# Kernel tuning notes

Measured on AMD Instinct MI355X. Metric: run time of the kernel, lower is better.

The kernel has to match this reference:

```python
import jax, jax.numpy as jnp
import numpy as np

POOL = 7
IMG = 1024.0
NUM_CLASSES = 2
R = 1000


def crop_and_resize(feat, boxes, pool):
    # feat: [C,H,W]; boxes: [N,4] normalized (y1,x1,y2,x2); returns [N,C,pool,pool]
    C, H, W = feat.shape
    y1, x1, y2, x2 = boxes[:, 0], boxes[:, 1], boxes[:, 2], boxes[:, 3]
    t = jnp.arange(pool, dtype=feat.dtype) / (pool - 1)
    ys = (y1[:, None] + (y2 - y1)[:, None] * t[None, :]) * (H - 1)  # [N,P]
    xs = (x1[:, None] + (x2 - x1)[:, None] * t[None, :]) * (W - 1)  # [N,P]
    vy = (ys >= 0) & (ys <= H - 1)
    vx = (xs >= 0) & (xs <= W - 1)
    yf = jnp.floor(ys)
    xf = jnp.floor(xs)
    wy = (ys - yf)[None, :, :, None]  # [1,N,P,1]
    wx = (xs - xf)[None, :, None, :]  # [1,N,1,P]
    y0 = jnp.clip(yf, 0, H - 1).astype(jnp.int32)
    y1i = jnp.clip(yf + 1, 0, H - 1).astype(jnp.int32)
    x0 = jnp.clip(xf, 0, W - 1).astype(jnp.int32)
    x1i = jnp.clip(xf + 1, 0, W - 1).astype(jnp.int32)

    def g(yi, xi):  # gather -> [C,N,P,P]
        return feat[:, yi[:, :, None], xi[:, None, :]]

    val = (g(y0, x0) * (1 - wy) * (1 - wx)
           + g(y0, x1i) * (1 - wy) * wx
           + g(y1i, x0) * wy * (1 - wx)
           + g(y1i, x1i) * wy * wx)
    mask = (vy[:, :, None] & vx[:, None, :])[None]  # extrapolation value 0
    return jnp.where(mask, val, 0.0).transpose(1, 0, 2, 3)


def roi_align(feats, rois_flat):
    # rois_flat: [N,4] in pixel coords (x1,y1,x2,y2)
    x1, y1, x2, y2 = rois_flat[:, 0], rois_flat[:, 1], rois_flat[:, 2], rois_flat[:, 3]
    lvl = jnp.log2(jnp.sqrt((y2 - y1) * (x2 - x1)) / 224.0)
    lvl = jnp.clip(jnp.round(lvl) + 4, 2, 5)
    boxes = rois_flat[:, jnp.array([1, 0, 3, 2])] / IMG  # (y1,x1,y2,x2) normalized
    crops = jnp.stack([crop_and_resize(f[0], boxes, POOL) for f in feats])  # [4,N,C,P,P]
    sel = (lvl[None, :] == jnp.arange(2, 6, dtype=lvl.dtype)[:, None])       # [4,N]
    return jnp.sum(jnp.where(sel[:, :, None, None, None], crops, 0.0), axis=0)  # [N,C,P,P]


def setup_inputs() -> dict:
    key = jax.random.key(0)
    ks = jax.random.split(key, 24)
    feat2 = jax.random.normal(ks[0], (1, 256, 256, 256), jnp.float32)
    feat3 = jax.random.normal(ks[1], (1, 256, 128, 128), jnp.float32)
    feat4 = jax.random.normal(ks[2], (1, 256, 64, 64), jnp.float32)
    feat5 = jax.random.normal(ks[3], (1, 256, 32, 32), jnp.float32)
    x1 = jax.random.uniform(ks[4], (1, R), minval=0.0, maxval=900.0)
    y1 = jax.random.uniform(ks[5], (1, R), minval=0.0, maxval=900.0)
    w = jax.random.uniform(ks[6], (1, R), minval=16.0, maxval=400.0)
    h = jax.random.uniform(ks[7], (1, R), minval=16.0, maxval=400.0)
    rois = jnp.stack([x1, y1, jnp.minimum(x1 + w, 1023.0), jnp.minimum(y1 + h, 1023.0)], axis=-1)
    s = 0.02
    params = dict(
        conv_w=s * jax.random.normal(ks[8], (1024, 256, POOL, POOL), jnp.float32),
        conv_b=jnp.zeros((1024,), jnp.float32),
        bn_gamma=jnp.ones((1024,), jnp.float32),
        bn_beta=jnp.zeros((1024,), jnp.float32),
        bn_mean=jnp.zeros((1024,), jnp.float32),
        bn_var=jnp.ones((1024,), jnp.float32),
        fc1_w=s * jax.random.normal(ks[9], (1024, 1024), jnp.float32),
        fc1_b=jnp.zeros((1024,), jnp.float32),
        fc2_w=s * jax.random.normal(ks[10], (1024, 1024), jnp.float32),
        fc2_b=jnp.zeros((1024,), jnp.float32),
        cls_w=s * jax.random.normal(ks[11], (NUM_CLASSES, 1024), jnp.float32),
        cls_b=jnp.zeros((NUM_CLASSES,), jnp.float32),
        bbox_w=s * jax.random.normal(ks[12], (NUM_CLASSES * 4, 1024), jnp.float32),
        bbox_b=jnp.zeros((NUM_CLASSES * 4,), jnp.float32),
    )
    return dict(feat2=feat2, feat3=feat3, feat4=feat4, feat5=feat5, rois=rois, **params)


def reference(feat2, feat3, feat4, feat5, rois, conv_w, conv_b, bn_gamma, bn_beta,
              bn_mean, bn_var, fc1_w, fc1_b, fc2_w, fc2_b, cls_w, cls_b, bbox_w, bbox_b):
    roi_number = rois.shape[1]
    pooled = roi_align([feat2, feat3, feat4, feat5], rois.reshape(-1, 4))  # [N,256,7,7]
    # conv1 (7x7 valid on 7x7 input -> 1x1 spatial) + BN (inference stats, eps=1e-3)
    y = jnp.einsum('nchw,ochw->no', pooled, conv_w) + conv_b
    y = (y - bn_mean) / jnp.sqrt(bn_var + 1e-3) * bn_gamma + bn_beta
    h = jax.nn.relu(y @ fc1_w.T + fc1_b)
    h = jax.nn.relu(h @ fc2_w.T + fc2_b)
    logits = h @ cls_w.T + cls_b
    probs = jax.nn.softmax(logits, axis=-1)
    bbox = h @ bbox_w.T + bbox_b
    return (logits.reshape(1, roi_number, NUM_CLASSES),
            probs.reshape(1, roi_number, NUM_CLASSES),
            bbox.reshape(1, roi_number, NUM_CLASSES, 4))
```

## Files before the change

### kernel.cpp

```cpp
#include <hip/hip_runtime.h>
#include <cstdint>
#include <cstddef>

typedef __attribute__((ext_vector_type(8))) short bf16x8;
typedef __attribute__((ext_vector_type(4))) float f32x4;

#define POOLK 12544

#define TOFF2 0
#define TOFF3 16777216
#define TOFF4 20971520
#define TOFF5 22020096

__device__ __forceinline__ void gld16(const void* g, void* l) {
    __builtin_amdgcn_global_load_lds(
        (const __attribute__((address_space(1))) void*)g,
        (__attribute__((address_space(3))) void*)l, 16, 0, 0);
}
__device__ __forceinline__ unsigned short f32_to_bf16(float f) {
    union { float f; unsigned u; } x; x.f = f;
    return (unsigned short)((x.u + 0x7FFFu + ((x.u >> 16) & 1u)) >> 16);
}
__device__ __forceinline__ float bf16_to_f32(unsigned short s) {
    return __uint_as_float(((unsigned)s) << 16);
}

__global__ __launch_bounds__(256) void prep_kernel(
    const float* __restrict__ f2, const float* __restrict__ f3,
    const float* __restrict__ f4, const float* __restrict__ f5,
    unsigned short* __restrict__ T,
    const float* __restrict__ conv_w, unsigned short* __restrict__ convw_bf,
    const float* __restrict__ fc1_w, unsigned short* __restrict__ fc1w_bf,
    const float* __restrict__ fc2_w, unsigned short* __restrict__ fc2w_bf,
    int do_feat)
{
    __shared__ __align__(16) unsigned short sh[8192];
    const int t = threadIdx.x;
    int b = blockIdx.x;

    if (b < 2720) {
        if (!do_feat) return;
        const float* src; unsigned short* dst; int P;
        if (b < 2048)      { src = f2; dst = T + TOFF2; P = 65536; }
        else if (b < 2560) { src = f3; dst = T + TOFF3; P = 16384; b -= 2048; }
        else if (b < 2688) { src = f4; dst = T + TOFF4; P = 4096;  b -= 2560; }
        else               { src = f5; dst = T + TOFF5; P = 1024;  b -= 2688; }
        const int p0 = b * 32;
        const int cr = t >> 3, x4 = (t & 7) * 4;
#pragma unroll
        for (int cc = 0; cc < 8; ++cc) {
            const int c = cc * 32 + cr;
            const float4 v = *(const float4*)(src + (size_t)c * P + p0 + x4);
            const int blk = c >> 3, cl = c & 7;
            float vv[4] = {v.x, v.y, v.z, v.w};
#pragma unroll
            for (int i = 0; i < 4; ++i) {
                const int p = x4 + i;
                sh[p * 256 + ((blk ^ (p >> 2)) << 3) + cl] = f32_to_bf16(vv[i]);
            }
        }
        __syncthreads();
        const int cb = t & 31;
#pragma unroll
        for (int pz = 0; pz < 4; ++pz) {
            const int pp = pz * 8 + (t >> 5);
            const bf16x8 v = *(const bf16x8*)&sh[pp * 256 + ((cb ^ (pp >> 2)) << 3)];
            *(bf16x8*)(dst + (size_t)(p0 + pp) * 256 + cb * 8) = v;
        }
        return;
    }
    b -= 2720;
    if (b < 2048) {
        const int o = b >> 1, half = b & 1;
        const float* srow = conv_w + (size_t)o * POOLK + half * 6272;
        for (int k = t; k < 6272; k += 256) sh[k] = f32_to_bf16(srow[k]);
        __syncthreads();
        unsigned short* drow = convw_bf + (size_t)o * POOLK + half * 128;
        for (int k = t; k < 6272; k += 256) {
            const int ij = k >> 7, cl = k & 127;
            drow[ij * 256 + cl] = sh[cl * 49 + ij];
        }
        return;
    }
    b -= 2048;
    {
        const float* src = (b < 1024) ? fc1_w : fc2_w;
        unsigned short* dst = (b < 1024) ? fc1w_bf : fc2w_bf;
        const int bb = b & 1023;
        const int i = (bb * 256 + t) * 4;
        const float4 v = *(const float4*)(src + i);
        ushort4 o;
        o.x = f32_to_bf16(v.x); o.y = f32_to_bf16(v.y);
        o.z = f32_to_bf16(v.z); o.w = f32_to_bf16(v.w);
        *(ushort4*)(dst + i) = o;
    }
}

__global__ __launch_bounds__(256) void roi_gather_kernel(
    const unsigned short* __restrict__ T, const float* __restrict__ rois,
    unsigned short* __restrict__ pooled, int nroi)
{
    const int n = blockIdx.x;
    const int tid = threadIdx.x;
    unsigned short* orow = pooled + (size_t)n * POOLK;
    if (n >= nroi) {
        const bf16x8 z = {};
        for (int k = tid * 8; k < POOLK; k += 2048) *(bf16x8*)(orow + k) = z;
        return;
    }
    __shared__ int sy0[7], sy1[7], sx0[7], sx1[7];
    __shared__ float swy[7], swx[7], svy[7], svx[7];

    const float rx1 = rois[n*4+0], ry1 = rois[n*4+1];
    const float rx2 = rois[n*4+2], ry2 = rois[n*4+3];
    int lvl = (int)rintf(log2f(sqrtf((ry2-ry1)*(rx2-rx1)) * (1.0f/224.0f))) + 4;
    lvl = lvl < 2 ? 2 : (lvl > 5 ? 5 : lvl);
    const int W = 256 >> (lvl - 2);
    const float Hm1 = (float)(W - 1);
    const unsigned short* Tl = T + (lvl == 2 ? TOFF2 : (lvl == 3 ? TOFF3 : (lvl == 4 ? TOFF4 : TOFF5)));

    if (tid < 7) {
        const float t = (float)tid / 6.0f;
        const float by1 = ry1*(1.0f/1024.0f), by2 = ry2*(1.0f/1024.0f);
        const float bx1 = rx1*(1.0f/1024.0f), bx2 = rx2*(1.0f/1024.0f);
        const float ys = (by1 + (by2 - by1) * t) * Hm1;
        const float xs = (bx1 + (bx2 - bx1) * t) * Hm1;
        const float yf = floorf(ys), xf = floorf(xs);
        swy[tid] = ys - yf;  swx[tid] = xs - xf;
        sy0[tid] = (int)fminf(fmaxf(yf,        0.0f), Hm1);
        sy1[tid] = (int)fminf(fmaxf(yf + 1.0f, 0.0f), Hm1);
        sx0[tid] = (int)fminf(fmaxf(xf,        0.0f), Hm1);
        sx1[tid] = (int)fminf(fmaxf(xf + 1.0f, 0.0f), Hm1);
        svy[tid] = (ys >= 0.0f && ys <= Hm1) ? 1.0f : 0.0f;
        svx[tid] = (xs >= 0.0f && xs <= Hm1) ? 1.0f : 0.0f;
    }
    __syncthreads();

    const int g  = tid >> 5;
    const int c0 = (tid & 31) * 8;
#pragma unroll
    for (int it = 0; it < 7; ++it) {
        const int pos = it * 8 + g;
        if (pos >= 49) break;
        const int i = pos / 7, j = pos % 7;
        const int y0 = sy0[i], y1 = sy1[i], x0 = sx0[j], x1 = sx1[j];
        const float wy = swy[i], wx = swx[j];
        const float scale = svy[i] * svx[j];
        const bf16x8 v00 = *(const bf16x8*)(Tl + ((size_t)(y0*W + x0))*256 + c0);
        const bf16x8 v01 = *(const bf16x8*)(Tl + ((size_t)(y0*W + x1))*256 + c0);
        const bf16x8 v10 = *(const bf16x8*)(Tl + ((size_t)(y1*W + x0))*256 + c0);
        const bf16x8 v11 = *(const bf16x8*)(Tl + ((size_t)(y1*W + x1))*256 + c0);
        bf16x8 o;
#pragma unroll
        for (int jj = 0; jj < 8; ++jj) {
            const float f00 = bf16_to_f32((unsigned short)v00[jj]);
            const float f01 = bf16_to_f32((unsigned short)v01[jj]);
            const float f10 = bf16_to_f32((unsigned short)v10[jj]);
            const float f11 = bf16_to_f32((unsigned short)v11[jj]);
            const float top = f00 + (f01 - f00) * wx;
            const float bot = f10 + (f11 - f10) * wx;
            o[jj] = (short)f32_to_bf16((top + (bot - top) * wy) * scale);
        }
        *(bf16x8*)(orow + pos * 256 + c0) = o;
    }
}

__global__ __launch_bounds__(256) void roi_direct_kernel(
    const float* __restrict__ feat2, const float* __restrict__ feat3,
    const float* __restrict__ feat4, const float* __restrict__ feat5,
    const float* __restrict__ rois, unsigned short* __restrict__ pooled, int nroi)
{
    const int n = blockIdx.x;
    const int tid = threadIdx.x;
    unsigned short* orow = pooled + (size_t)n * POOLK;
    if (n >= nroi) {
        const bf16x8 z = {};
        for (int k = tid * 8; k < POOLK; k += 2048) *(bf16x8*)(orow + k) = z;
        return;
    }
    __shared__ int sy0[7], sy1[7], sx0[7], sx1[7];
    __shared__ float swy[7], swx[7], svy[7], svx[7];
    const float rx1 = rois[n*4+0], ry1 = rois[n*4+1];
    const float rx2 = rois[n*4+2], ry2 = rois[n*4+3];
    int lvl = (int)rintf(log2f(sqrtf((ry2-ry1)*(rx2-rx1)) * (1.0f/224.0f))) + 4;
    lvl = lvl < 2 ? 2 : (lvl > 5 ? 5 : lvl);
    const int H = 256 >> (lvl - 2);
    const float Hm1 = (float)(H - 1);
    const float* feat = lvl==2 ? feat2 : (lvl==3 ? feat3 : (lvl==4 ? feat4 : feat5));
    if (tid < 7) {
        const float t = (float)tid / 6.0f;
        const float by1 = ry1*(1.0f/1024.0f), by2 = ry2*(1.0f/1024.0f);
        const float bx1 = rx1*(1.0f/1024.0f), bx2 = rx2*(1.0f/1024.0f);
        const float ys = (by1 + (by2-by1)*t) * Hm1;
        const float xs = (bx1 + (bx2-bx1)*t) * Hm1;
        const float yf = floorf(ys), xf = floorf(xs);
        swy[tid] = ys - yf;  swx[tid] = xs - xf;
        sy0[tid] = (int)fminf(fmaxf(yf,      0.0f), Hm1);
        sy1[tid] = (int)fminf(fmaxf(yf+1.0f, 0.0f), Hm1);
        sx0[tid] = (int)fminf(fmaxf(xf,      0.0f), Hm1);
        sx1[tid] = (int)fminf(fmaxf(xf+1.0f, 0.0f), Hm1);
        svy[tid] = (ys >= 0.0f && ys <= Hm1) ? 1.0f : 0.0f;
        svx[tid] = (xs >= 0.0f && xs <= Hm1) ? 1.0f : 0.0f;
    }
    __syncthreads();
    const int HW = H * H;
    for (int e = tid; e < POOLK; e += 256) {
        const int c = e / 49, ij = e % 49, i = ij / 7, j = ij % 7;
        const float* p = feat + c * HW;
        const int y0 = sy0[i], y1 = sy1[i], x0 = sx0[j], x1 = sx1[j];
        const float wy = swy[i], wx = swx[j];
        const float v00 = p[y0*H + x0], v01 = p[y0*H + x1];
        const float v10 = p[y1*H + x0], v11 = p[y1*H + x1];
        float v = v00*(1.0f-wy)*(1.0f-wx) + v01*(1.0f-wy)*wx
                + v10*wy*(1.0f-wx)        + v11*wy*wx;
        v *= svy[i] * svx[j];
        orow[ij*256 + c] = f32_to_bf16(v);
    }
}

__global__ __launch_bounds__(256, 2) void gemm_bt(
    const unsigned short* __restrict__ A, const unsigned short* __restrict__ B,
    float* __restrict__ Cpart, int K, int Kper, int nz)
{
    __shared__ __align__(16) unsigned short At[2][128*32];
    __shared__ __align__(16) unsigned short Bt[2][128*32];
    const int tid  = threadIdx.x;
    const int lane = tid & 63;
    const int bid  = blockIdx.x;
    const int z  = bid % nz;
    const int iq = bid / nz;
    const int bx = iq & 7, by = iq >> 3;
    const int wm = (tid >> 6) >> 1, wn = (tid >> 6) & 1;
    const size_t k0 = (size_t)z * Kper;

    const int r1 = tid >> 2;
    const int q  = tid & 3;
    const int csw = (q ^ (r1 & 3)) * 8;
    const unsigned short* Ag = A + ((size_t)(by * 128 + r1)) * K + k0 + csw;
    const unsigned short* Bg = B + ((size_t)(bx * 128 + r1)) * K + k0 + csw;
    const int nit = Kper >> 5;

    gld16(Ag,                  &At[0][tid * 8]);
    gld16(Ag + (size_t)64 * K, &At[0][(tid + 256) * 8]);
    gld16(Bg,                  &Bt[0][tid * 8]);
    gld16(Bg + (size_t)64 * K, &Bt[0][(tid + 256) * 8]);

    f32x4 acc[4][4] = {};
    const int fr = lane & 15;
    const int fq = lane >> 4;
    const int rslot = (fq ^ (fr & 3)) * 8;

    int buf = 0;
    for (int it = 0; it < nit; ++it) {
        if (it + 1 < nit) {
            const size_t ko = (size_t)(it + 1) * 32;
            gld16(Ag + ko,                  &At[buf ^ 1][tid * 8]);
            gld16(Ag + (size_t)64 * K + ko, &At[buf ^ 1][(tid + 256) * 8]);
            gld16(Bg + ko,                  &Bt[buf ^ 1][tid * 8]);
            gld16(Bg + (size_t)64 * K + ko, &Bt[buf ^ 1][(tid + 256) * 8]);
            asm volatile("s_waitcnt vmcnt(4)" ::: "memory");
        } else {
            asm volatile("s_waitcnt vmcnt(0)" ::: "memory");
        }
        __syncthreads();

        bf16x8 a[4], b[4];
#pragma unroll
        for (int mi = 0; mi < 4; ++mi)
            a[mi] = *(const bf16x8*)&At[buf][(wm*64 + mi*16 + fr) * 32 + rslot];
#pragma unroll
        for (int ni = 0; ni < 4; ++ni)
            b[ni] = *(const bf16x8*)&Bt[buf][(wn*64 + ni*16 + fr) * 32 + rslot];
        __builtin_amdgcn_s_setprio(1);
#pragma unroll
        for (int mi = 0; mi < 4; ++mi)
#pragma unroll
            for (int ni = 0; ni < 4; ++ni)
                acc[mi][ni] = __builtin_amdgcn_mfma_f32_16x16x32_bf16(
                    a[mi], b[ni], acc[mi][ni], 0, 0, 0);
        __builtin_amdgcn_s_setprio(0);
        __syncthreads();
        buf ^= 1;
    }

    float* Cp = Cpart + (size_t)z * (1024 * 1024);
    const int row0 = by * 128 + wm * 64;
    const int col0 = bx * 128 + wn * 64;
#pragma unroll
    for (int mi = 0; mi < 4; ++mi)
#pragma unroll
        for (int ni = 0; ni < 4; ++ni)
#pragma unroll
            for (int r = 0; r < 4; ++r)
                Cp[(size_t)(row0 + mi*16 + fq*4 + r) * 1024 + col0 + ni*16 + fr]
                    = acc[mi][ni][r];
}

__global__ void reduce_bn_kernel(const float* __restrict__ part,
    const float* __restrict__ bias, const float* __restrict__ gamma,
    const float* __restrict__ beta, const float* __restrict__ mean,
    const float* __restrict__ var, unsigned short* __restrict__ out, int nz)
{
    const int i4 = (blockIdx.x * 256 + threadIdx.x) * 4;
    const int n = i4 & 1023;
    float4 v = make_float4(0.f, 0.f, 0.f, 0.f);
    for (int zz = 0; zz < nz; ++zz) {
        const float4 p = *(const float4*)(part + (size_t)zz * 1048576 + i4);
        v.x += p.x; v.y += p.y; v.z += p.z; v.w += p.w;
    }
    const float4 bi = *(const float4*)(bias + n);
    const float4 ga = *(const float4*)(gamma + n);
    const float4 be = *(const float4*)(beta + n);
    const float4 me = *(const float4*)(mean + n);
    const float4 va = *(const float4*)(var + n);
    ushort4 o;
    o.x = f32_to_bf16((v.x + bi.x - me.x) * __frsqrt_rn(va.x + 0.001f) * ga.x + be.x);
    o.y = f32_to_bf16((v.y + bi.y - me.y) * __frsqrt_rn(va.y + 0.001f) * ga.y + be.y);
    o.z = f32_to_bf16((v.z + bi.z - me.z) * __frsqrt_rn(va.z + 0.001f) * ga.z + be.z);
    o.w = f32_to_bf16((v.w + bi.w - me.w) * __frsqrt_rn(va.w + 0.001f) * ga.w + be.w);
    *(ushort4*)(out + i4) = o;
}

__global__ __launch_bounds__(256) void gemm64_fused(
    const unsigned short* __restrict__ A, const unsigned short* __restrict__ B,
    const float* __restrict__ bias, unsigned short* __restrict__ out, int relu)
{
    __shared__ __align__(16) unsigned short At[2][64*32];
    __shared__ __align__(16) unsigned short Bt[2][64*32];
    const int tid = threadIdx.x, lane = tid & 63;
    const int w = tid >> 6, wm = w >> 1, wn = w & 1;
    const int r1 = tid >> 2;
    const int q  = tid & 3;
    const int csw = (q ^ (r1 & 3)) * 8;
    const unsigned short* Ag = A + (size_t)(blockIdx.y*64 + r1) * 1024 + csw;
    const unsigned short* Bg = B + (size_t)(blockIdx.x*64 + r1) * 1024 + csw;
    const int fr = lane & 15, fq = lane >> 4;
    const int rslot = (fq ^ (fr & 3)) * 8;

    gld16(Ag, &At[0][tid * 8]);
    gld16(Bg, &Bt[0][tid * 8]);

    f32x4 acc[2][2] = {};
    int buf = 0;
    for (int it = 0; it < 32; ++it) {
        if (it + 1 < 32) {
            const int ko = (it + 1) * 32;
            gld16(Ag + ko, &At[buf ^ 1][tid * 8]);
            gld16(Bg + ko, &Bt[buf ^ 1][tid * 8]);
            asm volatile("s_waitcnt vmcnt(2)" ::: "memory");
        } else {
            asm volatile("s_waitcnt vmcnt(0)" ::: "memory");
        }
        __syncthreads();
        bf16x8 a[2], b[2];
#pragma unroll
        for (int mi = 0; mi < 2; ++mi)
            a[mi] = *(const bf16x8*)&At[buf][(wm*32 + mi*16 + fr) * 32 + rslot];
#pragma unroll
        for (int ni = 0; ni < 2; ++ni)
            b[ni] = *(const bf16x8*)&Bt[buf][(wn*32 + ni*16 + fr) * 32 + rslot];
        __builtin_amdgcn_s_setprio(1);
#pragma unroll
        for (int mi = 0; mi < 2; ++mi)
#pragma unroll
            for (int ni = 0; ni < 2; ++ni)
                acc[mi][ni] = __builtin_amdgcn_mfma_f32_16x16x32_bf16(
                    a[mi], b[ni], acc[mi][ni], 0, 0, 0);
        __builtin_amdgcn_s_setprio(0);
        __syncthreads();
        buf ^= 1;
    }
    const int row0 = blockIdx.y*64 + wm*32;
    const int col0 = blockIdx.x*64 + wn*32;
#pragma unroll
    for (int mi = 0; mi < 2; ++mi)
#pragma unroll
        for (int ni = 0; ni < 2; ++ni)
#pragma unroll
            for (int r = 0; r < 4; ++r) {
                const int row = row0 + mi*16 + fq*4 + r;
                const int col = col0 + ni*16 + fr;
                float v = acc[mi][ni][r] + bias[col];
                if (relu) v = fmaxf(v, 0.0f);
                out[(size_t)row * 1024 + col] = f32_to_bf16(v);
            }
}

__global__ __launch_bounds__(256) void head_kernel(
    const unsigned short* __restrict__ h2,
    const float* __restrict__ cls_w, const float* __restrict__ cls_b,
    const float* __restrict__ bbox_w, const float* __restrict__ bbox_b,
    float* __restrict__ out)
{
    const int roi = blockIdx.x * 4 + (threadIdx.x >> 6);
    const int lane = threadIdx.x & 63;
    const unsigned short* hrow = h2 + (size_t)roi * 1024;
    float hv[16];
#pragma unroll
    for (int j = 0; j < 16; ++j)
        hv[j] = bf16_to_f32(hrow[lane*16 + j]);
    float r[10];
#pragma unroll
    for (int o = 0; o < 10; ++o) {
        const float* w = (o < 2) ? (cls_w + o*1024) : (bbox_w + (size_t)(o-2)*1024);
        float s = 0.f;
#pragma unroll
        for (int j = 0; j < 16; ++j) s += hv[j] * w[lane*16 + j];
#pragma unroll
        for (int off = 32; off > 0; off >>= 1) s += __shfl_xor(s, off);
        r[o] = s;
    }
    if (lane == 0) {
        const float l0 = r[0] + cls_b[0], l1 = r[1] + cls_b[1];
        out[roi*2+0] = l0; out[roi*2+1] = l1;
        const float m = fmaxf(l0, l1);
        const float e0 = expf(l0 - m), e1 = expf(l1 - m);
        const float inv = 1.0f / (e0 + e1);
        out[2000 + roi*2 + 0] = e0 * inv;
        out[2000 + roi*2 + 1] = e1 * inv;
#pragma unroll
        for (int qq = 0; qq < 8; ++qq) out[4000 + roi*8 + qq] = r[2+qq] + bbox_b[qq];
    }
}

extern "C" void kernel_launch(void* const* d_in, const int* in_sizes, int n_in,
                              void* d_out, int out_size, void* d_ws, size_t ws_size,
                              hipStream_t stream)
{
    const float* feat2   = (const float*)d_in[0];
    const float* feat3   = (const float*)d_in[1];
    const float* feat4   = (const float*)d_in[2];
    const float* feat5   = (const float*)d_in[3];
    const float* rois    = (const float*)d_in[4];
    const float* conv_w  = (const float*)d_in[5];
    const float* conv_b  = (const float*)d_in[6];
    const float* bn_gamma= (const float*)d_in[7];
    const float* bn_beta = (const float*)d_in[8];
    const float* bn_mean = (const float*)d_in[9];
    const float* bn_var  = (const float*)d_in[10];
    const float* fc1_w   = (const float*)d_in[11];
    const float* fc1_b   = (const float*)d_in[12];
    const float* fc2_w   = (const float*)d_in[13];
    const float* fc2_b   = (const float*)d_in[14];
    const float* cls_w   = (const float*)d_in[15];
    const float* cls_b   = (const float*)d_in[16];
    const float* bbox_w  = (const float*)d_in[17];
    const float* bbox_b  = (const float*)d_in[18];
    float* out = (float*)d_out;
    const int nroi = in_sizes[4] / 4;

    const size_t fixedBytes = (size_t)25690112 + 25690112 + 5 * (size_t)2097152;
    const size_t needA = fixedBytes + (size_t)44564480;
    const int tier = (ws_size >= needA) ? 1 : 2;
    const size_t regionA = tier == 1 ? (size_t)44564480 : (size_t)16777216;
    const int nzc  = tier == 1 ? 8 : 4;
    const int Kper = tier == 1 ? 1568 : 3136;

    char* ws = (char*)d_ws;
    size_t off = 0;
    auto alloc = [&](size_t bytes) {
        void* p = ws + off; off += (bytes + 255) & ~(size_t)255; return p;
    };
    char* rA = (char*)alloc(regionA);
    unsigned short* T    = (unsigned short*)rA;
    float*          part = (float*)rA;
    unsigned short* pooled   = (unsigned short*)alloc((size_t)1024 * POOLK * 2);
    unsigned short* convw_bf = (unsigned short*)alloc((size_t)1024 * POOLK * 2);
    unsigned short* fc1w_bf  = (unsigned short*)alloc((size_t)1048576 * 2);
    unsigned short* fc2w_bf  = (unsigned short*)alloc((size_t)1048576 * 2);
    unsigned short* ybf      = (unsigned short*)alloc((size_t)1048576 * 2);
    unsigned short* h1bf     = (unsigned short*)alloc((size_t)1048576 * 2);
    unsigned short* h2bf     = (unsigned short*)alloc((size_t)1048576 * 2);

    hipLaunchKernelGGL(prep_kernel, dim3(6816), dim3(256), 0, stream,
                       feat2, feat3, feat4, feat5, T,
                       conv_w, convw_bf, fc1_w, fc1w_bf, fc2_w, fc2w_bf,
                       tier == 1 ? 1 : 0);

    if (tier == 1) {
        hipLaunchKernelGGL(roi_gather_kernel, dim3(1024), dim3(256), 0, stream,
                           T, rois, pooled, nroi);
    } else {
        hipLaunchKernelGGL(roi_direct_kernel, dim3(1024), dim3(256), 0, stream,
                           feat2, feat3, feat4, feat5, rois, pooled, nroi);
    }

    hipLaunchKernelGGL(gemm_bt, dim3(64 * nzc), dim3(256), 0, stream,
                       pooled, convw_bf, part, POOLK, Kper, nzc);
    hipLaunchKernelGGL(reduce_bn_kernel, dim3(1024), dim3(256), 0, stream,
                       part, conv_b, bn_gamma, bn_beta, bn_mean, bn_var, ybf, nzc);

    hipLaunchKernelGGL(gemm64_fused, dim3(16, 16), dim3(256), 0, stream,
                       ybf, fc1w_bf, fc1_b, h1bf, 1);
    hipLaunchKernelGGL(gemm64_fused, dim3(16, 16), dim3(256), 0, stream,
                       h1bf, fc2w_bf, fc2_b, h2bf, 1);

    hipLaunchKernelGGL(head_kernel, dim3(250), dim3(256), 0, stream,
                       h2bf, cls_w, cls_b, bbox_w, bbox_b, out);
}
```

Measured before the change: 128.1 us.

## Split feature transpose out and fuse weight prep into ROI gather kernel

The single prep kernel is split so that the feature-map NCHW-to-NHWC bf16 transpose runs in its own kernel with larger 128-pixel tiles and a 64KB shared buffer. The weight conversions (conv, fc1, fc2) now run inside the ROI gather launch as extra blocks, so they overlap with gathering and one launch is removed. The fc conversion uses 16 elements per thread. The larger shared tile may lower occupancy in the transpose, and the mixed block types in the fused kernel could cause imbalance.

Result: slower. 131.4 us (+2.5%).

```diff
diff --git a/kernel.cpp b/kernel.cpp
--- a/kernel.cpp
+++ b/kernel.cpp
@@ -25,87 +25,99 @@
     return __uint_as_float(((unsigned)s) << 16);
 }
 
-__global__ __launch_bounds__(256) void prep_kernel(
+__global__ __launch_bounds__(256) void feat_tr_kernel(
     const float* __restrict__ f2, const float* __restrict__ f3,
     const float* __restrict__ f4, const float* __restrict__ f5,
-    unsigned short* __restrict__ T,
+    unsigned short* __restrict__ T)
+{
+    __shared__ __align__(16) unsigned short sh[128 * 256];
+    int b = blockIdx.x;
+    const float* src; unsigned short* dst; int P;
+    if (b < 512)      { src = f2; dst = T + TOFF2; P = 65536; }
+    else if (b < 640) { src = f3; dst = T + TOFF3; P = 16384; b -= 512; }
+    else if (b < 672) { src = f4; dst = T + TOFF4; P = 4096;  b -= 640; }
+    else              { src = f5; dst = T + TOFF5; P = 1024;  b -= 672; }
+    const int p0 = b * 128;
+    const int t = threadIdx.x;
+    const int lane5 = t & 31;
+    const int x4 = lane5 * 4;
+    const int fx = (lane5 & 7) << 3;
+
+#pragma unroll
+    for (int it = 0; it < 8; ++it) {
+        float4 v[4];
+        int cs[4];
+#pragma unroll
+        for (int u = 0; u < 4; ++u) {
+            cs[u] = it * 32 + u * 8 + (t >> 5);
+            v[u] = *(const float4*)(src + (size_t)cs[u] * P + p0 + x4);
+        }
+#pragma unroll
+        for (int u = 0; u < 4; ++u) {
+            const int cp = cs[u] ^ fx;
+            float vv[4] = {v[u].x, v[u].y, v[u].z, v[u].w};
+#pragma unroll
+            for (int i = 0; i < 4; ++i)
+                sh[(x4 + i) * 256 + cp] = f32_to_bf16(vv[i]);
+        }
+    }
+    __syncthreads();
+
+    const int c0 = lane5 * 8;
+#pragma unroll
+    for (int oz = 0; oz < 16; ++oz) {
+        const int pp = oz * 8 + (t >> 5);
+        const int cr = c0 ^ (((pp >> 2) & 7) << 3);
+        const bf16x8 vv = *(const bf16x8*)&sh[pp * 256 + cr];
+        *(bf16x8*)(dst + (size_t)(p0 + pp) * 256 + c0) = vv;
+    }
+}
+
+__global__ __launch_bounds__(256) void gather_prep_kernel(
+    const unsigned short* __restrict__ T, const float* __restrict__ rois,
+    unsigned short* __restrict__ pooled, int nroi,
     const float* __restrict__ conv_w, unsigned short* __restrict__ convw_bf,
     const float* __restrict__ fc1_w, unsigned short* __restrict__ fc1w_bf,
-    const float* __restrict__ fc2_w, unsigned short* __restrict__ fc2w_bf,
-    int do_feat)
-{
-    __shared__ __align__(16) unsigned short sh[8192];
+    const float* __restrict__ fc2_w, unsigned short* __restrict__ fc2w_bf)
+{
     const int t = threadIdx.x;
     int b = blockIdx.x;
 
-    if (b < 2720) {
-        if (!do_feat) return;
-        const float* src; unsigned short* dst; int P;
-        if (b < 2048)      { src = f2; dst = T + TOFF2; P = 65536; }
-        else if (b < 2560) { src = f3; dst = T + TOFF3; P = 16384; b -= 2048; }
-        else if (b < 2688) { src = f4; dst = T + TOFF4; P = 4096;  b -= 2560; }
-        else               { src = f5; dst = T + TOFF5; P = 1024;  b -= 2688; }
-        const int p0 = b * 32;
-        const int cr = t >> 3, x4 = (t & 7) * 4;
-#pragma unroll
-        for (int cc = 0; cc < 8; ++cc) {
-            const int c = cc * 32 + cr;
-            const float4 v = *(const float4*)(src + (size_t)c * P + p0 + x4);
-            const int blk = c >> 3, cl = c & 7;
-            float vv[4] = {v.x, v.y, v.z, v.w};
-#pragma unroll
-            for (int i = 0; i < 4; ++i) {
-                const int p = x4 + i;
-                sh[p * 256 + ((blk ^ (p >> 2)) << 3) + cl] = f32_to_bf16(vv[i]);
+    if (b >= 1024) {
+        b -= 1024;
+        if (b < 2048) {
+            __shared__ unsigned short sh[6272];
+            const int o = b >> 1, half = b & 1;
+            const float* srow = conv_w + (size_t)o * POOLK + half * 6272;
+            for (int k = t; k < 6272; k += 256) sh[k] = f32_to_bf16(srow[k]);
+            __syncthreads();
+            unsigned short* drow = convw_bf + (size_t)o * POOLK + half * 128;
+            for (int k = t; k < 6272; k += 256) {
+                const int ij = k >> 7, cl = k & 127;
+                drow[ij * 256 + cl] = sh[cl * 49 + ij];
             }
-        }
-        __syncthreads();
-        const int cb = t & 31;
-#pragma unroll
-        for (int pz = 0; pz < 4; ++pz) {
-            const int pp = pz * 8 + (t >> 5);
-            const bf16x8 v = *(const bf16x8*)&sh[pp * 256 + ((cb ^ (pp >> 2)) << 3)];
-            *(bf16x8*)(dst + (size_t)(p0 + pp) * 256 + cb * 8) = v;
+        } else {
+            b -= 2048;
+            const float* src = (b < 256) ? fc1_w : fc2_w;
+            unsigned short* dst = (b < 256) ? fc1w_bf : fc2w_bf;
+            const int base = (b & 255) * 4096 + t * 16;
+#pragma unroll
+            for (int u = 0; u < 4; ++u) {
+                const float4 v = *(const float4*)(src + base + u * 4);
+                ushort4 o4;
+                o4.x = f32_to_bf16(v.x); o4.y = f32_to_bf16(v.y);
+                o4.z = f32_to_bf16(v.z); o4.w = f32_to_bf16(v.w);
+                *(ushort4*)(dst + base + u * 4) = o4;
+            }
         }
         return;
     }
-    b -= 2720;
-    if (b < 2048) {
-        const int o = b >> 1, half = b & 1;
-        const float* srow = conv_w + (size_t)o * POOLK + half * 6272;
-        for (int k = t; k < 6272; k += 256) sh[k] = f32_to_bf16(srow[k]);
-        __syncthreads();
-        unsigned short* drow = convw_bf + (size_t)o * POOLK + half * 128;
-        for (int k = t; k < 6272; k += 256) {
-            const int ij = k >> 7, cl = k & 127;
-            drow[ij * 256 + cl] = sh[cl * 49 + ij];
-        }
-        return;
-    }
-    b -= 2048;
-    {
-        const float* src = (b < 1024) ? fc1_w : fc2_w;
-        unsigned short* dst = (b < 1024) ? fc1w_bf : fc2w_bf;
-        const int bb = b & 1023;
-        const int i = (bb * 256 + t) * 4;
-        const float4 v = *(const float4*)(src + i);
-        ushort4 o;
-        o.x = f32_to_bf16(v.x); o.y = f32_to_bf16(v.y);
-        o.z = f32_to_bf16(v.z); o.w = f32_to_bf16(v.w);
-        *(ushort4*)(dst + i) = o;
-    }
-}
-
-__global__ __launch_bounds__(256) void roi_gather_kernel(
-    const unsigned short* __restrict__ T, const float* __restrict__ rois,
-    unsigned short* __restrict__ pooled, int nroi)
-{
-    const int n = blockIdx.x;
-    const int tid = threadIdx.x;
+
+    const int n = b;
     unsigned short* orow = pooled + (size_t)n * POOLK;
     if (n >= nroi) {
         const bf16x8 z = {};
-        for (int k = tid * 8; k < POOLK; k += 2048) *(bf16x8*)(orow + k) = z;
+        for (int k = t * 8; k < POOLK; k += 2048) *(bf16x8*)(orow + k) = z;
         return;
     }
     __shared__ int sy0[7], sy1[7], sx0[7], sx1[7];
@@ -119,25 +131,25 @@
     const float Hm1 = (float)(W - 1);
     const unsigned short* Tl = T + (lvl == 2 ? TOFF2 : (lvl == 3 ? TOFF3 : (lvl == 4 ? TOFF4 : TOFF5)));
 
-    if (tid < 7) {
-        const float t = (float)tid / 6.0f;
+    if (t < 7) {
+        const float tt = (float)t / 6.0f;
         const float by1 = ry1*(1.0f/1024.0f), by2 = ry2*(1.0f/1024.0f);
         const float bx1 = rx1*(1.0f/1024.0f), bx2 = rx2*(1.0f/1024.0f);
-        const float ys = (by1 + (by2 - by1) * t) * Hm1;
-        const float xs = (bx1 + (bx2 - bx1) * t) * Hm1;
+        const float ys = (by1 + (by2 - by1) * tt) * Hm1;
+        const float xs = (bx1 + (bx2 - bx1) * tt) * Hm1;
         const float yf = floorf(ys), xf = floorf(xs);
-        swy[tid] = ys - yf;  swx[tid] = xs - xf;
-        sy0[tid] = (int)fminf(fmaxf(yf,        0.0f), Hm1);
-        sy1[tid] = (int)fminf(fmaxf(yf + 1.0f, 0.0f), Hm1);
-        sx0[tid] = (int)fminf(fmaxf(xf,        0.0f), Hm1);
-        sx1[tid] = (int)fminf(fmaxf(xf + 1.0f, 0.0f), Hm1);
-        svy[tid] = (ys >= 0.0f && ys <= Hm1) ? 1.0f : 0.0f;
-        svx[tid] = (xs >= 0.0f && xs <= Hm1) ? 1.0f : 0.0f;
+        swy[t] = ys - yf;  swx[t] = xs - xf;
+        sy0[t] = (int)fminf(fmaxf(yf,        0.0f), Hm1);
+        sy1[t] = (int)fminf(fmaxf(yf + 1.0f, 0.0f), Hm1);
+        sx0[t] = (int)fminf(fmaxf(xf,        0.0f), Hm1);
+        sx1[t] = (int)fminf(fmaxf(xf + 1.0f, 0.0f), Hm1);
+        svy[t] = (ys >= 0.0f && ys <= Hm1) ? 1.0f : 0.0f;
+        svx[t] = (xs >= 0.0f && xs <= Hm1) ? 1.0f : 0.0f;
     }
     __syncthreads();
 
-    const int g  = tid >> 5;
-    const int c0 = (tid & 31) * 8;
+    const int g  = t >> 5;
+    const int c0 = (t & 31) * 8;
 #pragma unroll
     for (int it = 0; it < 7; ++it) {
         const int pos = it * 8 + g;
@@ -218,6 +230,40 @@
     }
 }
 
+__global__ __launch_bounds__(256) void wprep_kernel(
+    const float* __restrict__ conv_w, unsigned short* __restrict__ convw_bf,
+    const float* __restrict__ fc1_w, unsigned short* __restrict__ fc1w_bf,
+    const float* __restrict__ fc2_w, unsigned short* __restrict__ fc2w_bf)
+{
+    const int t = threadIdx.x;
+    int b = blockIdx.x;
+    if (b < 2048) {
+        __shared__ unsigned short sh[6272];
+        const int o = b >> 1, half = b & 1;
+        const float* srow = conv_w + (size_t)o * POOLK + half * 6272;
+        for (int k = t; k < 6272; k += 256) sh[k] = f32_to_bf16(srow[k]);
+        __syncthreads();
+        unsigned short* drow = convw_bf + (size_t)o * POOLK + half * 128;
+        for (int k = t; k < 6272; k += 256) {
+            const int ij = k >> 7, cl = k & 127;
+            drow[ij * 256 + cl] = sh[cl * 49 + ij];
+        }
+        return;
+    }
+    b -= 2048;
+    const float* src = (b < 256) ? fc1_w : fc2_w;
+    unsigned short* dst = (b < 256) ? fc1w_bf : fc2w_bf;
+    const int base = (b & 255) * 4096 + t * 16;
+#pragma unroll
+    for (int u = 0; u < 4; ++u) {
+        const float4 v = *(const float4*)(src + base + u * 4);
+        ushort4 o4;
+        o4.x = f32_to_bf16(v.x); o4.y = f32_to_bf16(v.y);
+        o4.z = f32_to_bf16(v.z); o4.w = f32_to_bf16(v.w);
+        *(ushort4*)(dst + base + u * 4) = o4;
+    }
+}
+
 __global__ __launch_bounds__(256, 2) void gemm_bt(
     const unsigned short* __restrict__ A, const unsigned short* __restrict__ B,
     float* __restrict__ Cpart, int K, int Kper, int nz)
@@ -472,15 +518,15 @@
     unsigned short* h1bf     = (unsigned short*)alloc((size_t)1048576 * 2);
     unsigned short* h2bf     = (unsigned short*)alloc((size_t)1048576 * 2);
 
-    hipLaunchKernelGGL(prep_kernel, dim3(6816), dim3(256), 0, stream,
-                       feat2, feat3, feat4, feat5, T,
-                       conv_w, convw_bf, fc1_w, fc1w_bf, fc2_w, fc2w_bf,
-                       tier == 1 ? 1 : 0);
-
     if (tier == 1) {
-        hipLaunchKernelGGL(roi_gather_kernel, dim3(1024), dim3(256), 0, stream,
-                           T, rois, pooled, nroi);
+        hipLaunchKernelGGL(feat_tr_kernel, dim3(680), dim3(256), 0, stream,
+                           feat2, feat3, feat4, feat5, T);
+        hipLaunchKernelGGL(gather_prep_kernel, dim3(3584), dim3(256), 0, stream,
+                           T, rois, pooled, nroi,
+                           conv_w, convw_bf, fc1_w, fc1w_bf, fc2_w, fc2w_bf);
     } else {
+        hipLaunchKernelGGL(wprep_kernel, dim3(2560), dim3(256), 0, stream,
+                           conv_w, convw_bf, fc1_w, fc1w_bf, fc2_w, fc2w_bf);
         hipLaunchKernelGGL(roi_direct_kernel, dim3(1024), dim3(256), 0, stream,
                            feat2, feat3, feat4, feat5, rois, pooled, nroi);
     }
```
